# Kernel tuning notes

Hardware: AMD Instinct MI355X
Metric: run time of the kernel (lower is better)

Reference implementation:

```python
import jax, jax.numpy as jnp
import numpy as np

N_NODES = 50000
N_EDGES = 800000
IN_FEATS = 64
HIDDEN = 64
NUM_CLASSES = 32


def _graph_conv(x, src, dst, W, b, n_nodes):
    # DGL GraphConv, norm='both', allow_zero_in_degree=True:
    # out = D_in^{-1/2} * (A^T @ (D_out^{-1/2} * x)) @ W + b, degrees clamped to >=1
    e = src.shape[0]
    ones = jnp.ones((e,), dtype=x.dtype)
    out_deg = jax.ops.segment_sum(ones, src, num_segments=n_nodes)
    in_deg = jax.ops.segment_sum(ones, dst, num_segments=n_nodes)
    norm_src = jax.lax.rsqrt(jnp.maximum(out_deg, 1.0))[:, None]
    norm_dst = jax.lax.rsqrt(jnp.maximum(in_deg, 1.0))[:, None]
    h = x * norm_src                                   # [N, d]
    agg = jax.ops.segment_sum(h[src], dst, num_segments=n_nodes)  # gather+scatter over edges
    return (agg * norm_dst) @ W + b


def setup_inputs() -> dict:
    key = jax.random.key(0)
    k1, k2, k3, k4, k5 = jax.random.split(key, 5)
    features = jax.random.normal(k1, (N_NODES, IN_FEATS), dtype=jnp.float32)
    src = jax.random.randint(k2, (N_EDGES,), 0, N_NODES, dtype=jnp.int32)
    dst = jax.random.randint(k3, (N_EDGES,), 0, N_NODES, dtype=jnp.int32)
    W1 = jax.random.normal(k4, (IN_FEATS, HIDDEN), dtype=jnp.float32) * (1.0 / np.sqrt(IN_FEATS))
    b1 = jnp.zeros((HIDDEN,), dtype=jnp.float32)
    W2 = jax.random.normal(k5, (HIDDEN, NUM_CLASSES), dtype=jnp.float32) * (1.0 / np.sqrt(HIDDEN))
    b2 = jnp.zeros((NUM_CLASSES,), dtype=jnp.float32)
    return {"features": features, "src": src, "dst": dst,
            "W1": W1, "b1": b1, "W2": W2, "b2": b2}


def reference(features, src, dst, W1, b1, W2, b2) -> jnp.ndarray:
    n = features.shape[0]
    h = jax.nn.relu(_graph_conv(features, src, dst, W1, b1, n))
    out = _graph_conv(h, src, dst, W2, b2, n)
    # single canonical etype -> mean over one-element stack is identity
    return out
```

## Files before the change

### kernel.cpp

```cpp
#include <hip/hip_runtime.h>
#include <hip/hip_bf16.h>

#define N_NODES 50000
#define N_EDGES 800000
#define F 64
#define C 32
#define CAP 48

#define NPB   200
#define EPB   4000
#define NBUCK 196

static __device__ __forceinline__ float bf2f(unsigned short u) {
    return __uint_as_float(((unsigned)u) << 16);
}
static __device__ __forceinline__ unsigned short f2bf(float f) {
    __hip_bfloat16 h = __float2bfloat16(f);
    return *reinterpret_cast<unsigned short*>(&h);
}

__global__ void part_count_kernel(const int* __restrict__ src, const int* __restrict__ dst,
                                  int* __restrict__ bcnt_d, int* __restrict__ bcnt_s) {
    __shared__ int hd[NBUCK], hs[NBUCK];
    int t = threadIdx.x;
    for (int i = t; i < NBUCK; i += 256) { hd[i] = 0; hs[i] = 0; }
    __syncthreads();
    int b0 = blockIdx.x * EPB;
    for (int i = b0 + t; i < b0 + EPB; i += 256) {
        atomicAdd(&hd[dst[i] >> 8], 1);
        atomicAdd(&hs[src[i] >> 8], 1);
    }
    __syncthreads();
    for (int i = t; i < NBUCK; i += 256) {
        bcnt_d[blockIdx.x * NBUCK + i] = hd[i];
        bcnt_s[blockIdx.x * NBUCK + i] = hs[i];
    }
}

__global__ void part_scan_kernel(const int* __restrict__ bcnt_d, const int* __restrict__ bcnt_s,
                                 int* __restrict__ eoff_d, int* __restrict__ eoff_s,
                                 int* __restrict__ base_d, int* __restrict__ base_s) {
    __shared__ int tot_d[NBUCK], tot_s[NBUCK], bd[NBUCK + 1], bs[NBUCK + 1];
    int t = threadIdx.x;
    if (t < NBUCK) {
        int run = 0;
        for (int blk = 0; blk < NPB; blk++) {
            eoff_d[blk * NBUCK + t] = run;
            run += bcnt_d[blk * NBUCK + t];
        }
        tot_d[t] = run;
        run = 0;
        for (int blk = 0; blk < NPB; blk++) {
            eoff_s[blk * NBUCK + t] = run;
            run += bcnt_s[blk * NBUCK + t];
        }
        tot_s[t] = run;
    }
    __syncthreads();
    if (t == 0) {
        int r = 0;
        for (int b = 0; b < NBUCK; b++) { bd[b] = r; r += tot_d[b]; }
        bd[NBUCK] = r;
        r = 0;
        for (int b = 0; b < NBUCK; b++) { bs[b] = r; r += tot_s[b]; }
        bs[NBUCK] = r;
    }
    __syncthreads();
    if (t < NBUCK + 1) { base_d[t] = bd[t]; base_s[t] = bs[t]; }
}

__global__ void part_scatter_kernel(const int* __restrict__ src, const int* __restrict__ dst,
                                    const int* __restrict__ eoff_d, const int* __restrict__ eoff_s,
                                    const int* __restrict__ base_d, const int* __restrict__ base_s,
                                    int* __restrict__ edge_d, int* __restrict__ edge_s) {
    __shared__ int cd[NBUCK], cs[NBUCK];
    int t = threadIdx.x;
    for (int i = t; i < NBUCK; i += 256) {
        cd[i] = base_d[i] + eoff_d[blockIdx.x * NBUCK + i];
        cs[i] = base_s[i] + eoff_s[blockIdx.x * NBUCK + i];
    }
    __syncthreads();
    int b0 = blockIdx.x * EPB;
    for (int i = b0 + t; i < b0 + EPB; i += 256) {
        int d = dst[i], s = src[i];
        int p = atomicAdd(&cd[d >> 8], 1);
        edge_d[p] = ((d & 255) << 16) | s;
        int q = atomicAdd(&cs[s >> 8], 1);
        edge_s[q] = s & 255;
    }
}

__global__ void bucket_build_kernel(const int* __restrict__ edge_d, const int* __restrict__ edge_s,
                                    const int* __restrict__ base_d, const int* __restrict__ base_s,
                                    int* __restrict__ csr, int* __restrict__ cnt,
                                    float* __restrict__ norm_dst, float* __restrict__ norm_src) {
    __shared__ int cur[256];
    __shared__ int hs[256];
    int t = threadIdx.x;
    int bucket = blockIdx.x;
    cur[t] = 0;
    hs[t] = 0;
    __syncthreads();
    int lo = base_d[bucket], hi = base_d[bucket + 1];
    for (int i = lo + t; i < hi; i += 256) {
        int pd = edge_d[i];
        int dlow = pd >> 16;
        int s = pd & 0xFFFF;
        int pos = atomicAdd(&cur[dlow], 1);
        if (pos < CAP) csr[(size_t)(bucket * 256 + dlow) * CAP + pos] = s;
    }
    int slo = base_s[bucket], shi = base_s[bucket + 1];
    for (int i = slo + t; i < shi; i += 256) {
        atomicAdd(&hs[edge_s[i]], 1);
    }
    __syncthreads();
    int node = bucket * 256 + t;
    if (node < N_NODES) {
        int c = cur[t] < CAP ? cur[t] : CAP;
        cnt[node] = c;
        norm_dst[node] = rsqrtf(fmaxf((float)c, 1.0f));
        norm_src[node] = rsqrtf(fmaxf((float)hs[t], 1.0f));
    }
}

__global__ void gemm_y_kernel(const float* __restrict__ x,
                              const float* __restrict__ ns,
                              const float* __restrict__ W,
                              __hip_bfloat16* __restrict__ y) {
    __shared__ float sW[F * F];
    __shared__ float srow[16][F];
    int t = threadIdx.x;
    for (int i = t; i < F * F; i += 256) sW[i] = W[i];
    int j = t & 63;
    int w = t >> 6;
    int base = blockIdx.x * 16;
    for (int r = w; r < 16; r += 4) srow[r][j] = x[(size_t)(base + r) * F + j];
    __syncthreads();
    float a0 = 0, a1 = 0, a2 = 0, a3 = 0;
#pragma unroll
    for (int k = 0; k < F; k++) {
        float wv = sW[k * F + j];
        a0 += srow[w * 4 + 0][k] * wv;
        a1 += srow[w * 4 + 1][k] * wv;
        a2 += srow[w * 4 + 2][k] * wv;
        a3 += srow[w * 4 + 3][k] * wv;
    }
    int n0 = base + w * 4;
    y[(size_t)(n0 + 0) * F + j] = __float2bfloat16(a0 * ns[n0 + 0]);
    y[(size_t)(n0 + 1) * F + j] = __float2bfloat16(a1 * ns[n0 + 1]);
    y[(size_t)(n0 + 2) * F + j] = __float2bfloat16(a2 * ns[n0 + 2]);
    y[(size_t)(n0 + 3) * F + j] = __float2bfloat16(a3 * ns[n0 + 3]);
}

struct f4 { float x, y, z, w; };
struct f2 { float x, y; };

static __device__ __forceinline__ void gacc(const __hip_bfloat16* __restrict__ tab,
                                            int s, int fo, f4& a) {
    const ushort4 v = *reinterpret_cast<const ushort4*>(
        reinterpret_cast<const unsigned short*>(tab) + (size_t)s * F + fo);
    a.x += bf2f(v.x); a.y += bf2f(v.y); a.z += bf2f(v.z); a.w += bf2f(v.w);
}
static __device__ __forceinline__ void gacc2(const unsigned short* __restrict__ tab,
                                             int s, int fo, f2& a) {
    const ushort2 v = *reinterpret_cast<const ushort2*>(tab + (size_t)s * C + fo);
    a.x += bf2f(v.x); a.y += bf2f(v.y);
}

__global__ void gather64_gemv_kernel(const __hip_bfloat16* __restrict__ y,
                                     const int* __restrict__ csr,
                                     const int* __restrict__ cnt,
                                     const float* __restrict__ norm_dst,
                                     const float* __restrict__ norm_src,
                                     const float* __restrict__ b1,
                                     const float* __restrict__ W2,
                                     __hip_bfloat16* __restrict__ gt) {
    __shared__ float sW[F * C];
    __shared__ float sagg[4][F];
    int t = threadIdx.x;
    for (int i = t; i < F * C; i += 256) sW[i] = W2[i];
    int w    = t >> 6;
    int lane = t & 63;
    int node = blockIdx.x * 4 + w;
    int g  = lane >> 4;
    int fo = (lane & 15) * 4;
    int n = cnt[node];
    const int* row = csr + (size_t)node * CAP;
    f4 a = {0.f, 0.f, 0.f, 0.f};
    int e = 0;
    if (e + 15 < n) {
        int4 idx = *reinterpret_cast<const int4*>(row + e + 4 * g);
        for (; e + 31 < n; e += 16) {
            int4 nxt = *reinterpret_cast<const int4*>(row + e + 16 + 4 * g);
            gacc(y, idx.x, fo, a);
            gacc(y, idx.y, fo, a);
            gacc(y, idx.z, fo, a);
            gacc(y, idx.w, fo, a);
            idx = nxt;
        }
        gacc(y, idx.x, fo, a);
        gacc(y, idx.y, fo, a);
        gacc(y, idx.z, fo, a);
        gacc(y, idx.w, fo, a);
        e += 16;
    }
    for (; e < n; e += 4) {
        int ee = e + g;
        if (ee < n) gacc(y, row[ee], fo, a);
    }
    a.x += __shfl_down(a.x, 16); a.y += __shfl_down(a.y, 16);
    a.z += __shfl_down(a.z, 16); a.w += __shfl_down(a.w, 16);
    a.x += __shfl_down(a.x, 32); a.y += __shfl_down(a.y, 32);
    a.z += __shfl_down(a.z, 32); a.w += __shfl_down(a.w, 32);
    if (lane < 16) {
        float nd = norm_dst[node], ns = norm_src[node];
        sagg[w][fo + 0] = fmaxf(a.x * nd + b1[fo + 0], 0.0f) * ns;
        sagg[w][fo + 1] = fmaxf(a.y * nd + b1[fo + 1], 0.0f) * ns;
        sagg[w][fo + 2] = fmaxf(a.z * nd + b1[fo + 2], 0.0f) * ns;
        sagg[w][fo + 3] = fmaxf(a.w * nd + b1[fo + 3], 0.0f) * ns;
    }
    __syncthreads();
    int j    = lane & 31;
    int half = lane >> 5;
    float o = 0.0f;
#pragma unroll
    for (int k = 0; k < 32; k++) {
        int kk = half * 32 + k;
        o += sagg[w][kk] * sW[kk * C + j];
    }
    o += __shfl_down(o, 32);
    if (half == 0)
        __builtin_nontemporal_store(f2bf(o),
            reinterpret_cast<unsigned short*>(gt) + (size_t)node * C + j);
}

__global__ void gather_out_kernel(const __hip_bfloat16* __restrict__ gt,
                                  const int* __restrict__ csr,
                                  const int* __restrict__ cnt,
                                  const float* __restrict__ norm_dst,
                                  const float* __restrict__ b2,
                                  float* __restrict__ out) {
    int gid  = blockIdx.x * blockDim.x + threadIdx.x;
    int node = gid >> 6;
    if (node >= N_NODES) return;
    int lane = threadIdx.x & 63;
    int g  = lane >> 4;
    int fo = (lane & 15) * 2;
    const unsigned short* tab = reinterpret_cast<const unsigned short*>(gt);
    int n = cnt[node];
    const int* row = csr + (size_t)node * CAP;
    f2 a = {0.f, 0.f};
    int e = 0;
    if (e + 15 < n) {
        int4 idx = *reinterpret_cast<const int4*>(row + e + 4 * g);
        for (; e + 31 < n; e += 16) {
            int4 nxt = *reinterpret_cast<const int4*>(row + e + 16 + 4 * g);
            gacc2(tab, idx.x, fo, a);
            gacc2(tab, idx.y, fo, a);
            gacc2(tab, idx.z, fo, a);
            gacc2(tab, idx.w, fo, a);
            idx = nxt;
        }
        gacc2(tab, idx.x, fo, a);
        gacc2(tab, idx.y, fo, a);
        gacc2(tab, idx.z, fo, a);
        gacc2(tab, idx.w, fo, a);
        e += 16;
    }
    for (; e < n; e += 4) {
        int ee = e + g;
        if (ee < n) gacc2(tab, row[ee], fo, a);
    }
    a.x += __shfl_down(a.x, 16); a.y += __shfl_down(a.y, 16);
    a.x += __shfl_down(a.x, 32); a.y += __shfl_down(a.y, 32);
    if (lane < 16) {
        float nd = norm_dst[node];
        float ox = a.x * nd + b2[fo + 0];
        float oy = a.y * nd + b2[fo + 1];
        unsigned long long pk = ((unsigned long long)__float_as_uint(ox)) |
                                ((unsigned long long)__float_as_uint(oy) << 32);
        __builtin_nontemporal_store(pk, reinterpret_cast<unsigned long long*>(
            out + (size_t)node * C + fo));
    }
}

extern "C" void kernel_launch(void* const* d_in, const int* in_sizes, int n_in,
                              void* d_out, int out_size, void* d_ws, size_t ws_size,
                              hipStream_t stream) {
    const float* features = (const float*)d_in[0];
    const int*   src      = (const int*)d_in[1];
    const int*   dst      = (const int*)d_in[2];
    const float* W1       = (const float*)d_in[3];
    const float* b1       = (const float*)d_in[4];
    const float* W2       = (const float*)d_in[5];
    const float* b2       = (const float*)d_in[6];
    float* out = (float*)d_out;

    char* p = (char*)d_ws;
    float* norm_src = (float*)p;  p += (size_t)N_NODES * 4;
    float* norm_dst = (float*)p;  p += (size_t)N_NODES * 4;
    int*   cnt      = (int*)p;    p += (size_t)N_NODES * 4;
    int*   csr      = (int*)p;    p += (size_t)N_NODES * CAP * 4;
    __hip_bfloat16* y  = (__hip_bfloat16*)p;  p += (size_t)N_NODES * F * 2;
    __hip_bfloat16* gt = (__hip_bfloat16*)p;

    int* edge_d = (int*)y;
    int* edge_s = edge_d + N_EDGES;
    int* q = (int*)gt;
    int* bcnt_d = q;                 q += NPB * NBUCK;
    int* bcnt_s = q;                 q += NPB * NBUCK;
    int* eoff_d = q;                 q += NPB * NBUCK;
    int* eoff_s = q;                 q += NPB * NBUCK;
    int* base_d = q;                 q += NBUCK + 1;
    int* base_s = q;

    part_count_kernel<<<NPB, 256, 0, stream>>>(src, dst, bcnt_d, bcnt_s);
    part_scan_kernel<<<1, 256, 0, stream>>>(bcnt_d, bcnt_s, eoff_d, eoff_s, base_d, base_s);
    part_scatter_kernel<<<NPB, 256, 0, stream>>>(src, dst, eoff_d, eoff_s, base_d, base_s,
                                                 edge_d, edge_s);
    bucket_build_kernel<<<NBUCK, 256, 0, stream>>>(edge_d, edge_s, base_d, base_s,
                                                   csr, cnt, norm_dst, norm_src);

    gemm_y_kernel<<<N_NODES / 16, 256, 0, stream>>>(features, norm_src, W1, y);
    gather64_gemv_kernel<<<N_NODES / 4, 256, 0, stream>>>(y, csr, cnt, norm_dst,
                                                          norm_src, b1, W2, gt);

    gather_out_kernel<<<(N_NODES * 64) / 256, 256, 0, stream>>>(gt, csr, cnt, norm_dst,
                                                                b2, out);
}
```

Baseline: 203.5 us.

## Rework gather kernels with 16-byte loads, branchless rounds, and persistent blocks

The two gather kernels now use 8 edge groups per wave with wider vector loads (8 bf16 or 4 bf16 per lane) and fixed unrolled rounds gated by degree, replacing the pipelined index loop. The first gather also becomes a grid-stride persistent kernel that does the GEMV through lane shuffles instead of shared memory. Partition counts are transposed so the scan reads contiguous int4 data, and edge_s is narrowed to bytes. Masked rounds always load row entries up to the cap, adding some wasted loads for low-degree nodes.

```diff
diff --git a/kernel.cpp b/kernel.cpp
--- a/kernel.cpp
+++ b/kernel.cpp
@@ -11,8 +11,13 @@
 #define EPB   4000
 #define NBUCK 196
 
-static __device__ __forceinline__ float bf2f(unsigned short u) {
+#define G1_BLOCKS 2048
+
+static __device__ __forceinline__ float bflo(int u) {
     return __uint_as_float(((unsigned)u) << 16);
+}
+static __device__ __forceinline__ float bfhi(int u) {
+    return __uint_as_float(((unsigned)u) & 0xffff0000u);
 }
 static __device__ __forceinline__ unsigned short f2bf(float f) {
     __hip_bfloat16 h = __float2bfloat16(f);
@@ -32,8 +37,8 @@
     }
     __syncthreads();
     for (int i = t; i < NBUCK; i += 256) {
-        bcnt_d[blockIdx.x * NBUCK + i] = hd[i];
-        bcnt_s[blockIdx.x * NBUCK + i] = hs[i];
+        bcnt_d[i * NPB + blockIdx.x] = hd[i];
+        bcnt_s[i * NPB + blockIdx.x] = hs[i];
     }
 }
 
@@ -44,15 +49,25 @@
     int t = threadIdx.x;
     if (t < NBUCK) {
         int run = 0;
-        for (int blk = 0; blk < NPB; blk++) {
-            eoff_d[blk * NBUCK + t] = run;
-            run += bcnt_d[blk * NBUCK + t];
+        for (int q = 0; q < NPB / 4; q++) {
+            int4 v = *reinterpret_cast<const int4*>(bcnt_d + t * NPB + 4 * q);
+            int4 o;
+            o.x = run; run += v.x;
+            o.y = run; run += v.y;
+            o.z = run; run += v.z;
+            o.w = run; run += v.w;
+            *reinterpret_cast<int4*>(eoff_d + t * NPB + 4 * q) = o;
         }
         tot_d[t] = run;
         run = 0;
-        for (int blk = 0; blk < NPB; blk++) {
-            eoff_s[blk * NBUCK + t] = run;
-            run += bcnt_s[blk * NBUCK + t];
+        for (int q = 0; q < NPB / 4; q++) {
+            int4 v = *reinterpret_cast<const int4*>(bcnt_s + t * NPB + 4 * q);
+            int4 o;
+            o.x = run; run += v.x;
+            o.y = run; run += v.y;
+            o.z = run; run += v.z;
+            o.w = run; run += v.w;
+            *reinterpret_cast<int4*>(eoff_s + t * NPB + 4 * q) = o;
         }
         tot_s[t] = run;
     }
@@ -72,12 +87,12 @@
 __global__ void part_scatter_kernel(const int* __restrict__ src, const int* __restrict__ dst,
                                     const int* __restrict__ eoff_d, const int* __restrict__ eoff_s,
                                     const int* __restrict__ base_d, const int* __restrict__ base_s,
-                                    int* __restrict__ edge_d, int* __restrict__ edge_s) {
+                                    int* __restrict__ edge_d, unsigned char* __restrict__ edge_s) {
     __shared__ int cd[NBUCK], cs[NBUCK];
     int t = threadIdx.x;
     for (int i = t; i < NBUCK; i += 256) {
-        cd[i] = base_d[i] + eoff_d[blockIdx.x * NBUCK + i];
-        cs[i] = base_s[i] + eoff_s[blockIdx.x * NBUCK + i];
+        cd[i] = base_d[i] + eoff_d[i * NPB + blockIdx.x];
+        cs[i] = base_s[i] + eoff_s[i * NPB + blockIdx.x];
     }
     __syncthreads();
     int b0 = blockIdx.x * EPB;
@@ -86,11 +101,12 @@
         int p = atomicAdd(&cd[d >> 8], 1);
         edge_d[p] = ((d & 255) << 16) | s;
         int q = atomicAdd(&cs[s >> 8], 1);
-        edge_s[q] = s & 255;
-    }
-}
-
-__global__ void bucket_build_kernel(const int* __restrict__ edge_d, const int* __restrict__ edge_s,
+        edge_s[q] = (unsigned char)(s & 255);
+    }
+}
+
+__global__ void bucket_build_kernel(const int* __restrict__ edge_d,
+                                    const unsigned char* __restrict__ edge_s,
                                     const int* __restrict__ base_d, const int* __restrict__ base_s,
                                     int* __restrict__ csr, int* __restrict__ cnt,
                                     float* __restrict__ norm_dst, float* __restrict__ norm_src) {
@@ -150,21 +166,6 @@
     y[(size_t)(n0 + 1) * F + j] = __float2bfloat16(a1 * ns[n0 + 1]);
     y[(size_t)(n0 + 2) * F + j] = __float2bfloat16(a2 * ns[n0 + 2]);
     y[(size_t)(n0 + 3) * F + j] = __float2bfloat16(a3 * ns[n0 + 3]);
-}
-
-struct f4 { float x, y, z, w; };
-struct f2 { float x, y; };
-
-static __device__ __forceinline__ void gacc(const __hip_bfloat16* __restrict__ tab,
-                                            int s, int fo, f4& a) {
-    const ushort4 v = *reinterpret_cast<const ushort4*>(
-        reinterpret_cast<const unsigned short*>(tab) + (size_t)s * F + fo);
-    a.x += bf2f(v.x); a.y += bf2f(v.y); a.z += bf2f(v.z); a.w += bf2f(v.w);
-}
-static __device__ __forceinline__ void gacc2(const unsigned short* __restrict__ tab,
-                                             int s, int fo, f2& a) {
-    const ushort2 v = *reinterpret_cast<const ushort2*>(tab + (size_t)s * C + fo);
-    a.x += bf2f(v.x); a.y += bf2f(v.y);
 }
 
 __global__ void gather64_gemv_kernel(const __hip_bfloat16* __restrict__ y,
@@ -176,62 +177,82 @@
                                      const float* __restrict__ W2,
                                      __hip_bfloat16* __restrict__ gt) {
     __shared__ float sW[F * C];
-    __shared__ float sagg[4][F];
     int t = threadIdx.x;
     for (int i = t; i < F * C; i += 256) sW[i] = W2[i];
+    __syncthreads();
     int w    = t >> 6;
     int lane = t & 63;
-    int node = blockIdx.x * 4 + w;
-    int g  = lane >> 4;
-    int fo = (lane & 15) * 4;
-    int n = cnt[node];
-    const int* row = csr + (size_t)node * CAP;
-    f4 a = {0.f, 0.f, 0.f, 0.f};
-    int e = 0;
-    if (e + 15 < n) {
-        int4 idx = *reinterpret_cast<const int4*>(row + e + 4 * g);
-        for (; e + 31 < n; e += 16) {
-            int4 nxt = *reinterpret_cast<const int4*>(row + e + 16 + 4 * g);
-            gacc(y, idx.x, fo, a);
-            gacc(y, idx.y, fo, a);
-            gacc(y, idx.z, fo, a);
-            gacc(y, idx.w, fo, a);
-            idx = nxt;
-        }
-        gacc(y, idx.x, fo, a);
-        gacc(y, idx.y, fo, a);
-        gacc(y, idx.z, fo, a);
-        gacc(y, idx.w, fo, a);
-        e += 16;
-    }
-    for (; e < n; e += 4) {
-        int ee = e + g;
-        if (ee < n) gacc(y, row[ee], fo, a);
-    }
-    a.x += __shfl_down(a.x, 16); a.y += __shfl_down(a.y, 16);
-    a.z += __shfl_down(a.z, 16); a.w += __shfl_down(a.w, 16);
-    a.x += __shfl_down(a.x, 32); a.y += __shfl_down(a.y, 32);
-    a.z += __shfl_down(a.z, 32); a.w += __shfl_down(a.w, 32);
-    if (lane < 16) {
-        float nd = norm_dst[node], ns = norm_src[node];
-        sagg[w][fo + 0] = fmaxf(a.x * nd + b1[fo + 0], 0.0f) * ns;
-        sagg[w][fo + 1] = fmaxf(a.y * nd + b1[fo + 1], 0.0f) * ns;
-        sagg[w][fo + 2] = fmaxf(a.z * nd + b1[fo + 2], 0.0f) * ns;
-        sagg[w][fo + 3] = fmaxf(a.w * nd + b1[fo + 3], 0.0f) * ns;
-    }
-    __syncthreads();
+    int g  = lane >> 3;
+    int fo = (lane & 7) * 8;
     int j    = lane & 31;
     int half = lane >> 5;
-    float o = 0.0f;
+    const float4 b1a = *reinterpret_cast<const float4*>(b1 + fo);
+    const float4 b1b = *reinterpret_cast<const float4*>(b1 + fo + 4);
+    const unsigned short* ytab = reinterpret_cast<const unsigned short*>(y);
+
+    for (int node = blockIdx.x * 4 + w; node < N_NODES; node += G1_BLOCKS * 4) {
+        int n = cnt[node];
+        const int* row = csr + (size_t)node * CAP;
+        float a0 = 0.f, a1 = 0.f, a2 = 0.f, a3 = 0.f,
+              a4 = 0.f, a5 = 0.f, a6 = 0.f, a7 = 0.f;
+
+#define G1_ROUND(i)                                                          \
+        {                                                                    \
+            int ee = (i) * 8 + g;                                            \
+            int rv = row[ee];                 \
+            int ss = (ee < n) ? rv : 0;                                      \
+            float m = (ee < n) ? 1.f : 0.f;                                  \
+            const int4 v = *reinterpret_cast<const int4*>(                   \
+                ytab + (size_t)ss * F + fo);                                 \
+            a0 = fmaf(m, bflo(v.x), a0); a1 = fmaf(m, bfhi(v.x), a1);        \
+            a2 = fmaf(m, bflo(v.y), a2); a3 = fmaf(m, bfhi(v.y), a3);        \
+            a4 = fmaf(m, bflo(v.z), a4); a5 = fmaf(m, bfhi(v.z), a5);        \
+            a6 = fmaf(m, bflo(v.w), a6); a7 = fmaf(m, bfhi(v.w), a7);        \
+        }
+        G1_ROUND(0)
+        G1_ROUND(1)
+        if (n > 16) {
+            G1_ROUND(2)
+            G1_ROUND(3)
+            if (n > 32) {
+                G1_ROUND(4)
+                G1_ROUND(5)
+            }
+        }
+#undef G1_ROUND
+
+#define G1_RED(mk)                                                           \
+        a0 += __shfl_xor(a0, mk); a1 += __shfl_xor(a1, mk);                  \
+        a2 += __shfl_xor(a2, mk); a3 += __shfl_xor(a3, mk);                  \
+        a4 += __shfl_xor(a4, mk); a5 += __shfl_xor(a5, mk);                  \
+        a6 += __shfl_xor(a6, mk); a7 += __shfl_xor(a7, mk);
+        G1_RED(8)
+        G1_RED(16)
+        G1_RED(32)
+#undef G1_RED
+
+        float nd = norm_dst[node], ns = norm_src[node];
+        float hh[8];
+        hh[0] = fmaxf(fmaf(a0, nd, b1a.x), 0.f) * ns;
+        hh[1] = fmaxf(fmaf(a1, nd, b1a.y), 0.f) * ns;
+        hh[2] = fmaxf(fmaf(a2, nd, b1a.z), 0.f) * ns;
+        hh[3] = fmaxf(fmaf(a3, nd, b1a.w), 0.f) * ns;
+        hh[4] = fmaxf(fmaf(a4, nd, b1b.x), 0.f) * ns;
+        hh[5] = fmaxf(fmaf(a5, nd, b1b.y), 0.f) * ns;
+        hh[6] = fmaxf(fmaf(a6, nd, b1b.z), 0.f) * ns;
+        hh[7] = fmaxf(fmaf(a7, nd, b1b.w), 0.f) * ns;
+
+        float o = 0.f;
 #pragma unroll
-    for (int k = 0; k < 32; k++) {
-        int kk = half * 32 + k;
-        o += sagg[w][kk] * sW[kk * C + j];
-    }
-    o += __shfl_down(o, 32);
-    if (half == 0)
-        __builtin_nontemporal_store(f2bf(o),
-            reinterpret_cast<unsigned short*>(gt) + (size_t)node * C + j);
+        for (int k = 0; k < 32; k++) {
+            float hv = __shfl(hh[k & 7], (half << 2) + (k >> 3));
+            o = fmaf(hv, sW[(half * 32 + k) * C + j], o);
+        }
+        o += __shfl_down(o, 32);
+        if (half == 0)
+            __builtin_nontemporal_store(f2bf(o),
+                reinterpret_cast<unsigned short*>(gt) + (size_t)node * C + j);
+    }
 }
 
 __global__ void gather_out_kernel(const __hip_bfloat16* __restrict__ gt,
@@ -240,47 +261,62 @@
                                   const float* __restrict__ norm_dst,
                                   const float* __restrict__ b2,
                                   float* __restrict__ out) {
-    int gid  = blockIdx.x * blockDim.x + threadIdx.x;
-    int node = gid >> 6;
-    if (node >= N_NODES) return;
-    int lane = threadIdx.x & 63;
-    int g  = lane >> 4;
-    int fo = (lane & 15) * 2;
+    int t = threadIdx.x;
+    int w = t >> 6;
+    int lane = t & 63;
+    int node = blockIdx.x * 4 + w;
+    int g  = lane >> 3;
+    int fo = (lane & 7) * 4;
     const unsigned short* tab = reinterpret_cast<const unsigned short*>(gt);
     int n = cnt[node];
     const int* row = csr + (size_t)node * CAP;
-    f2 a = {0.f, 0.f};
-    int e = 0;
-    if (e + 15 < n) {
-        int4 idx = *reinterpret_cast<const int4*>(row + e + 4 * g);
-        for (; e + 31 < n; e += 16) {
-            int4 nxt = *reinterpret_cast<const int4*>(row + e + 16 + 4 * g);
-            gacc2(tab, idx.x, fo, a);
-            gacc2(tab, idx.y, fo, a);
-            gacc2(tab, idx.z, fo, a);
-            gacc2(tab, idx.w, fo, a);
-            idx = nxt;
-        }
-        gacc2(tab, idx.x, fo, a);
-        gacc2(tab, idx.y, fo, a);
-        gacc2(tab, idx.z, fo, a);
-        gacc2(tab, idx.w, fo, a);
-        e += 16;
-    }
-    for (; e < n; e += 4) {
-        int ee = e + g;
-        if (ee < n) gacc2(tab, row[ee], fo, a);
-    }
-    a.x += __shfl_down(a.x, 16); a.y += __shfl_down(a.y, 16);
-    a.x += __shfl_down(a.x, 32); a.y += __shfl_down(a.y, 32);
-    if (lane < 16) {
+    float a0 = 0.f, a1 = 0.f, a2 = 0.f, a3 = 0.f;
+
+#define G2_ROUND(i)                                                          \
+    {                                                                        \
+        int ee = (i) * 8 + g;                                                \
+        int rv = row[ee];                                                    \
+        int ss = (ee < n) ? rv : 0;                                          \
+        float m = (ee < n) ? 1.f : 0.f;                                      \
+        const int2 v = *reinterpret_cast<const int2*>(                       \
+            tab + (size_t)ss * C + fo);                                      \
+        a0 = fmaf(m, bflo(v.x), a0); a1 = fmaf(m, bfhi(v.x), a1);            \
+        a2 = fmaf(m, bflo(v.y), a2); a3 = fmaf(m, bfhi(v.y), a3);            \
+    }
+    G2_ROUND(0)
+    G2_ROUND(1)
+    if (n > 16) {
+        G2_ROUND(2)
+        G2_ROUND(3)
+        if (n > 32) {
+            G2_ROUND(4)
+            G2_ROUND(5)
+        }
+    }
+#undef G2_ROUND
+
+    a0 += __shfl_xor(a0, 8);  a1 += __shfl_xor(a1, 8);
+    a2 += __shfl_xor(a2, 8);  a3 += __shfl_xor(a3, 8);
+    a0 += __shfl_xor(a0, 16); a1 += __shfl_xor(a1, 16);
+    a2 += __shfl_xor(a2, 16); a3 += __shfl_xor(a3, 16);
+    a0 += __shfl_xor(a0, 32); a1 += __shfl_xor(a1, 32);
+    a2 += __shfl_xor(a2, 32); a3 += __shfl_xor(a3, 32);
+
+    if (lane < 8) {
         float nd = norm_dst[node];
-        float ox = a.x * nd + b2[fo + 0];
-        float oy = a.y * nd + b2[fo + 1];
-        unsigned long long pk = ((unsigned long long)__float_as_uint(ox)) |
-                                ((unsigned long long)__float_as_uint(oy) << 32);
-        __builtin_nontemporal_store(pk, reinterpret_cast<unsigned long long*>(
-            out + (size_t)node * C + fo));
+        const float4 bb = *reinterpret_cast<const float4*>(b2 + fo);
+        float o0 = fmaf(a0, nd, bb.x);
+        float o1 = fmaf(a1, nd, bb.y);
+        float o2 = fmaf(a2, nd, bb.z);
+        float o3 = fmaf(a3, nd, bb.w);
+        unsigned long long p0 = ((unsigned long long)__float_as_uint(o0)) |
+                                ((unsigned long long)__float_as_uint(o1) << 32);
+        unsigned long long p1 = ((unsigned long long)__float_as_uint(o2)) |
+                                ((unsigned long long)__float_as_uint(o3) << 32);
+        unsigned long long* po = reinterpret_cast<unsigned long long*>(
+            out + (size_t)node * C + fo);
+        __builtin_nontemporal_store(p0, po);
+        __builtin_nontemporal_store(p1, po + 1);
     }
 }
 
@@ -305,7 +341,7 @@
     __hip_bfloat16* gt = (__hip_bfloat16*)p;
 
     int* edge_d = (int*)y;
-    int* edge_s = edge_d + N_EDGES;
+    unsigned char* edge_s = (unsigned char*)(edge_d + N_EDGES);
     int* q = (int*)gt;
     int* bcnt_d = q;                 q += NPB * NBUCK;
     int* bcnt_s = q;                 q += NPB * NBUCK;
@@ -322,9 +358,9 @@
                                                    csr, cnt, norm_dst, norm_src);
 
     gemm_y_kernel<<<N_NODES / 16, 256, 0, stream>>>(features, norm_src, W1, y);
-    gather64_gemv_kernel<<<N_NODES / 4, 256, 0, stream>>>(y, csr, cnt, norm_dst,
-                                                          norm_src, b1, W2, gt);
-
-    gather_out_kernel<<<(N_NODES * 64) / 256, 256, 0, stream>>>(gt, csr, cnt, norm_dst,
-                                                                b2, out);
-}
+    gather64_gemv_kernel<<<G1_BLOCKS, 256, 0, stream>>>(y, csr, cnt, norm_dst,
+                                                        norm_src, b1, W2, gt);
+
+    gather_out_kernel<<<N_NODES / 4, 256, 0, stream>>>(gt, csr, cnt, norm_dst,
+                                                       b2, out);
+}
```

Measured after the change: 209.5 us. +3.0%, slower.
